# Optimization experiments

Hardware: AMD Instinct MI355X
Metric: run time of the kernel (lower is better)

The kernel has to match this reference:

```python
import jax, jax.numpy as jnp
import numpy as np

N, E, F, H, T, K = 50000, 800000, 128, 128, 10, 3


def setup_inputs() -> dict:
    key = jax.random.key(0)
    ks = jax.random.split(key, 12)
    def p(k, shape):
        return jax.random.normal(k, shape, dtype=jnp.float32) * 0.05
    inp = {
        "x": jax.random.normal(ks[0], (N, F), dtype=jnp.float32),
        "edge_index": jax.random.randint(ks[1], (2, E), 0, N, dtype=jnp.int64),
        "edge_weight": jax.random.uniform(ks[2], (E,), dtype=jnp.float32),
    }
    names = ["xz", "hz", "xr", "hr", "xh", "hh"]
    for i, nm in enumerate(names):
        cin = F if nm[0] == "x" else H
        inp["W" + nm] = p(ks[3 + i], (K, cin, H))  # ChebConv: K linear maps [in,out]
        inp["b" + nm] = jnp.zeros((H,), jnp.float32)
    inp["Wlin"] = p(ks[9], (H, T))
    inp["blin"] = jnp.zeros((T,), jnp.float32)
    return inp


def _cheb_norm(src, dst, edge_weight, n):
    # PyG ChebConv norm with normalization='sym', lambda_max=2.0:
    # L_hat = 2L/lambda_max - I = -D^{-1/2} A D^{-1/2}  (zero diagonal)
    deg = jax.ops.segment_sum(edge_weight, src, num_segments=n)
    deg_safe = jnp.where(deg > 0, deg, 1.0)
    dinv = jnp.where(deg > 0, jax.lax.rsqrt(deg_safe), 0.0)
    return -dinv[src] * edge_weight * dinv[dst]


def _cheb_conv(x, W, b, src, dst, norm, n):
    # out = sum_k T_k(L_hat) x @ W[k] + b, via Chebyshev recurrence
    def prop(t):  # L_hat @ t : gather from source nodes, scatter-add into targets
        return jax.ops.segment_sum(norm[:, None] * t[src], dst, num_segments=n)
    Tx0 = x
    out = Tx0 @ W[0]
    Tx1 = prop(Tx0)
    out = out + Tx1 @ W[1]
    for k in range(2, W.shape[0]):
        Tx2 = 2.0 * prop(Tx1) - Tx0
        out = out + Tx2 @ W[k]
        Tx0, Tx1 = Tx1, Tx2
    return out + b


def reference(x, edge_index, edge_weight, Wxz, bxz, Whz, bhz, Wxr, bxr,
              Whr, bhr, Wxh, bxh, Whh, bhh, Wlin, blin):
    n = x.shape[0]
    src, dst = edge_index[0], edge_index[1]
    norm = _cheb_norm(src, dst, edge_weight, n)
    Hs = jnp.zeros((n, Whz.shape[2]), x.dtype)  # GConvGRU inits H=None -> zeros
    Z = jax.nn.sigmoid(_cheb_conv(x, Wxz, bxz, src, dst, norm, n)
                       + _cheb_conv(Hs, Whz, bhz, src, dst, norm, n))
    R = jax.nn.sigmoid(_cheb_conv(x, Wxr, bxr, src, dst, norm, n)
                       + _cheb_conv(Hs, Whr, bhr, src, dst, norm, n))
    Ht = jnp.tanh(_cheb_conv(x, Wxh, bxh, src, dst, norm, n)
                  + _cheb_conv(Hs * R, Whh, bhh, src, dst, norm, n))
    Hn = Z * Hs + (1.0 - Z) * Ht
    return Hn @ Wlin + blin
```

## Files before the change

### kernel.cpp

```cpp
#include <hip/hip_runtime.h>

typedef __attribute__((ext_vector_type(8))) short bf16x8;
typedef __attribute__((ext_vector_type(4))) float f32x4;
typedef unsigned int u32;
typedef unsigned short u16;

#define CAP 48

static __device__ __forceinline__ u16 f2bf(float f) {
  u32 u = __float_as_uint(f);
  u32 r = (u + 0x7fffu + ((u >> 16) & 1u)) >> 16;
  return (u16)r;
}
static __device__ __forceinline__ void gload16(const void* g, void* l) {
  __builtin_amdgcn_global_load_lds((const __attribute__((address_space(1))) u32*)g,
                                   (__attribute__((address_space(3))) u32*)l, 16, 0, 0);
}

__global__ __launch_bounds__(256) void deg_kernel(const int* __restrict__ ei,
                                                  const float* __restrict__ w,
                                                  float* __restrict__ deg, int E, int N) {
  int e = blockIdx.x * 256 + threadIdx.x;
  if (e >= E) return;
  int s = ei[e];
  if ((unsigned)s < (unsigned)N) atomicAdd(&deg[s], w[e]);
}

__global__ __launch_bounds__(256) void scatter_kernel(const int* __restrict__ ei,
                                                      const float* __restrict__ w,
                                                      const float* __restrict__ deg,
                                                      int* __restrict__ cur,
                                                      int2* __restrict__ edges, int E, int N) {
  int e = blockIdx.x * 256 + threadIdx.x;
  if (e >= E) return;
  int s = ei[e], d = ei[E + e];
  if ((unsigned)s < (unsigned)N && (unsigned)d < (unsigned)N) {
    float ds = deg[s], dd = deg[d];
    float is = ds > 0.f ? rsqrtf(ds) : 0.f;
    float id = dd > 0.f ? rsqrtf(dd) : 0.f;
    float nv = -is * w[e] * id;
    int pos = atomicAdd(&cur[d], 1);
    if (pos < CAP) edges[d * CAP + pos] = make_int2(s, __float_as_int(nv));
  }
}

__global__ __launch_bounds__(256) void convert_kernel(const float* __restrict__ x,
                                                      u32* __restrict__ xw, int nw) {
  int i = blockIdx.x * 256 + threadIdx.x;
  if (i < nw) {
    float2 v = *(const float2*)&x[(size_t)i * 2];
    xw[i] = (u32)f2bf(v.x) | ((u32)f2bf(v.y) << 16);
  }
}

#define ACC8(VV, NN)                                                    \
  _Pragma("unroll") for (int k_ = 0; k_ < 8; ++k_) {                    \
    a0 += NN[k_] * __uint_as_float(VV[k_] << 16);                       \
    a1 += NN[k_] * __uint_as_float(VV[k_] & 0xffff0000u);               \
  }

__global__ __launch_bounds__(256) void prop1_kernel(const u32* __restrict__ xw,
    const int2* __restrict__ edges, const int* __restrict__ cur,
    u32* __restrict__ t1w, int N) {
  int node = (blockIdx.x << 2) + (threadIdx.x >> 6);
  if (node >= N) return;
  int lane = threadIdx.x & 63;
  int len = cur[node]; if (len > CAP) len = CAP;
  int2 my = edges[node * CAP + (lane < CAP ? lane : CAP - 1)];
  float a0 = 0.f, a1 = 0.f;
  u32 v[8]; float nv[8];
#pragma unroll
  for (int k = 0; k < 8; ++k) {
    int s = __shfl(my.x, k);
    float n = __int_as_float(__shfl(my.y, k));
    if (k < len) { v[k] = xw[((unsigned)s << 6) | (unsigned)lane]; nv[k] = n; }
    else { v[k] = 0; nv[k] = 0.f; }
  }
  for (int base = 0; base < len; base += 8) {
    u32 vv[8]; float nn[8];
#pragma unroll
    for (int k = 0; k < 8; ++k) { vv[k] = v[k]; nn[k] = nv[k]; }
#pragma unroll
    for (int k = 0; k < 8; ++k) {
      int kn = base + 8 + k;
      int s = __shfl(my.x, kn);
      float n = __int_as_float(__shfl(my.y, kn));
      if (kn < len) { v[k] = xw[((unsigned)s << 6) | (unsigned)lane]; nv[k] = n; }
      else { v[k] = 0; nv[k] = 0.f; }
    }
    ACC8(vv, nn);
  }
  t1w[((unsigned)node << 6) | (unsigned)lane] = (u32)f2bf(a0) | ((u32)f2bf(a1) << 16);
}

__global__ __launch_bounds__(256) void prop2_kernel(const u32* __restrict__ xbw,
    const u32* __restrict__ xw ,
    const int2* __restrict__ edges, const int* __restrict__ cur,
    u32* __restrict__ t2w, int N) {
  int node = (blockIdx.x << 2) + (threadIdx.x >> 6);
  if (node >= N) return;
  int lane = threadIdx.x & 63;
  int len = cur[node]; if (len > CAP) len = CAP;
  int2 my = edges[node * CAP + (lane < CAP ? lane : CAP - 1)];
  float a0 = 0.f, a1 = 0.f;
  u32 v[8]; float nv[8];
#pragma unroll
  for (int k = 0; k < 8; ++k) {
    int s = __shfl(my.x, k);
    float n = __int_as_float(__shfl(my.y, k));
    if (k < len) { v[k] = xw[((unsigned)s << 6) | (unsigned)lane]; nv[k] = n; }
    else { v[k] = 0; nv[k] = 0.f; }
  }
  for (int base = 0; base < len; base += 8) {
    u32 vv[8]; float nn[8];
#pragma unroll
    for (int k = 0; k < 8; ++k) { vv[k] = v[k]; nn[k] = nv[k]; }
#pragma unroll
    for (int k = 0; k < 8; ++k) {
      int kn = base + 8 + k;
      int s = __shfl(my.x, kn);
      float n = __int_as_float(__shfl(my.y, kn));
      if (kn < len) { v[k] = xw[((unsigned)s << 6) | (unsigned)lane]; nv[k] = n; }
      else { v[k] = 0; nv[k] = 0.f; }
    }
    ACC8(vv, nn);
  }
  u32 xv = xbw[((unsigned)node << 6) | (unsigned)lane];
  float r0 = 2.f * a0 - __uint_as_float(xv << 16);
  float r1 = 2.f * a1 - __uint_as_float(xv & 0xffff0000u);
  t2w[((unsigned)node << 6) | (unsigned)lane] = (u32)f2bf(r0) | ((u32)f2bf(r1) << 16);
}

__global__ __launch_bounds__(256) void packB_kernel(const float* __restrict__ Wxz,
    const float* __restrict__ Wxh, const float* __restrict__ bxz, const float* __restrict__ bhz,
    const float* __restrict__ bxh, const float* __restrict__ bhh,
    u16* __restrict__ Bp, float* __restrict__ bzs, float* __restrict__ bhs) {
  int idx = blockIdx.x * 256 + threadIdx.x;
  int j = idx & 7, h4 = (idx >> 3) & 3, n = (idx >> 5) & 15, ct = (idx >> 9) & 15, kt = idx >> 13;
  int k = kt * 32 + h4 * 8 + j;
  int c = ct * 16 + n;
  int kb = k >> 7, ci = k & 127, h = c >> 1;
  const float* W = (c & 1) ? Wxh : Wxz;
  float v = W[((size_t)kb * 128 + ci) * 128 + h];
  Bp[idx] = f2bf(v);
  if (idx < 128) { bzs[idx] = bxz[idx] + bhz[idx]; bhs[idx] = bxh[idx] + bhh[idx]; }
}

__global__ __launch_bounds__(512, 2) void gemm_kernel(
    const u16* __restrict__ xb, const u16* __restrict__ t1, const u16* __restrict__ t2,
    const u16* __restrict__ Bp, const float* __restrict__ bzs, const float* __restrict__ bhs,
    const float* __restrict__ Wlin, const float* __restrict__ blin,
    float* __restrict__ out, int N) {
  __shared__ __align__(16) char smem[49152];
  const int offB_[2] = {0, 16384};
  const int offA_[2] = {32768, 40960};

  int tid = threadIdx.x;
  int w = tid >> 6, lane = tid & 63;
  int l15 = lane & 15, lh = lane >> 4;
  int rowBase = blockIdx.x << 7;
  int wrow = (w >> 2) << 6;
  int wcol = (w & 3) << 6;

  const u16* acts[3] = {xb, t1, t2};

  f32x4 acc[4][4];
  f32x4 zero = {0.f, 0.f, 0.f, 0.f};
#pragma unroll
  for (int mi = 0; mi < 4; ++mi)
#pragma unroll
    for (int ni = 0; ni < 4; ++ni) acc[mi][ni] = zero;

  auto stageB = [&](int kt, int buf) {
    const char* g = (const char*)Bp + kt * 16384 + w * 2048 + lane * 16;
    char* l = smem + offB_[buf] + w * 2048;
    gload16(g, l);
    gload16(g + 1024, l + 1024);
  };
  auto stageA = [&](int kt, int buf) {
    int kb = kt >> 2;
    const u16* act = acts[kb];
    int rl = (w << 4) + (lane >> 2);
    int grow = rowBase + rl; if (grow >= N) grow = N - 1;
    int hsw = (lane & 3) ^ ((rl >> 1) & 3);
    const char* g = (const char*)act + (size_t)grow * 256 + ((kt & 3) << 6) + (hsw << 4);
    char* l = smem + offA_[buf] + (w << 10);
    gload16(g, l);
  };

  stageB(0, 0); stageA(0, 0);

#pragma unroll
  for (int kt = 0; kt < 12; ++kt) {
    __syncthreads();
    if (kt < 11) { stageB(kt + 1, (kt + 1) & 1); stageA(kt + 1, (kt + 1) & 1); }
    const char* Ab = smem + offA_[kt & 1];
    const char* Bb = smem + offB_[kt & 1];
    bf16x8 a[4], b[4];
#pragma unroll
    for (int mi = 0; mi < 4; ++mi) {
      int row = wrow + (mi << 4) + l15;
      int off = (row << 6) + ((lh ^ ((row >> 1) & 3)) << 4);
      a[mi] = *(const bf16x8*)(Ab + off);
    }
#pragma unroll
    for (int ni = 0; ni < 4; ++ni) {
      int ct = ((w & 3) << 2) + ni;
      int off = (((ct << 4) + l15) << 6) + (lh << 4);
      b[ni] = *(const bf16x8*)(Bb + off);
    }
#pragma unroll
    for (int mi = 0; mi < 4; ++mi)
#pragma unroll
      for (int ni = 0; ni < 4; ++ni)
        acc[mi][ni] = __builtin_amdgcn_mfma_f32_16x16x32_bf16(a[mi], b[ni], acc[mi][ni], 0, 0, 0);
  }

  __syncthreads();

  u16* HnS = (u16*)smem;
  float* WlS = (float*)(smem + 34816);
  float* blS = (float*)(smem + 34816 + 5120);
  for (int i = tid; i < 1280; i += 512) WlS[i] = Wlin[i];
  if (tid < 10) blS[tid] = blin[tid];

  int odd = lane & 1;
#pragma unroll
  for (int ni = 0; ni < 4; ++ni) {
    int h = (wcol + (ni << 4) + l15) >> 1;
    float badd = odd ? bhs[h] : bzs[h];
#pragma unroll
    for (int mi = 0; mi < 4; ++mi)
#pragma unroll
      for (int reg = 0; reg < 4; ++reg) {
        float pre = acc[mi][ni][reg] + badd;
        float s2 = odd ? 2.f * pre : pre;
        float e = __expf(s2);
        float A = odd ? 1.f : 0.f;
        float B = odd ? 2.f : -1.f;
        float r = A - B / (1.f + e);
        float o = __shfl_xor(r, 1);
        if (!odd) {
          int row = wrow + (mi << 4) + (lh << 2) + reg;
          HnS[row * 136 + h] = f2bf(r * o);
        }
      }
  }
  __syncthreads();

  for (int idx = tid; idx < 1280; idx += 512) {
    int row = idx / 10, t = idx - row * 10;
    int grow = rowBase + row;
    if (grow < N) {
      float s = blS[t];
      const u16* hr = HnS + row * 136;
#pragma unroll 4
      for (int hc = 0; hc < 16; ++hc) {
        uint4 q = *(const uint4*)(hr + (hc << 3));
        const float* wp = WlS + (hc << 3) * 10 + t;
        s += __uint_as_float(q.x << 16) * wp[0];
        s += __uint_as_float(q.x & 0xffff0000u) * wp[10];
        s += __uint_as_float(q.y << 16) * wp[20];
        s += __uint_as_float(q.y & 0xffff0000u) * wp[30];
        s += __uint_as_float(q.z << 16) * wp[40];
        s += __uint_as_float(q.z & 0xffff0000u) * wp[50];
        s += __uint_as_float(q.w << 16) * wp[60];
        s += __uint_as_float(q.w & 0xffff0000u) * wp[70];
      }
      out[(size_t)grow * 10 + t] = s;
    }
  }
}

extern "C" void kernel_launch(void* const* d_in, const int* in_sizes, int n_in,
                              void* d_out, int out_size, void* d_ws, size_t ws_size,
                              hipStream_t stream) {
  const float* x    = (const float*)d_in[0];
  const int*   ei   = (const int*)d_in[1];
  const float* w    = (const float*)d_in[2];
  const float* Wxz  = (const float*)d_in[3];
  const float* bxz  = (const float*)d_in[4];
  const float* bhz  = (const float*)d_in[6];
  const float* Wxh  = (const float*)d_in[11];
  const float* bxh  = (const float*)d_in[12];
  const float* bhh  = (const float*)d_in[14];
  const float* Wlin = (const float*)d_in[15];
  const float* blin = (const float*)d_in[16];
  float* out = (float*)d_out;

  int N = in_sizes[0] / 128;
  int E = in_sizes[2];

  char* p = (char*)d_ws;
  auto alloc = [&](size_t bytes) {
    char* r = p;
    p += (bytes + 255) & ~(size_t)255;
    return r;
  };
  float* deg   = (float*)alloc((size_t)N * 4);
  int*   cur   = (int*)alloc((size_t)N * 4);
  int2*  edges = (int2*)alloc((size_t)N * CAP * 8);
  u32*   xbw   = (u32*)alloc((size_t)N * 256);
  u32*   t1w   = (u32*)alloc((size_t)N * 256);
  u32*   t2w   = (u32*)alloc((size_t)N * 256);
  u16*   Bp    = (u16*)alloc(196608);
  float* bzs   = (float*)alloc(512);
  float* bhs   = (float*)alloc(512);

  hipMemsetAsync(deg, 0, (size_t)N * 4, stream);
  hipMemsetAsync(cur, 0, (size_t)N * 4, stream);

  int eb = (E + 255) / 256;
  int nw = N * 64;
  hipLaunchKernelGGL(convert_kernel, dim3((nw + 255) / 256), dim3(256), 0, stream, x, xbw, nw);
  hipLaunchKernelGGL(packB_kernel, dim3(384), dim3(256), 0, stream,
                     Wxz, Wxh, bxz, bhz, bxh, bhh, Bp, bzs, bhs);
  hipLaunchKernelGGL(deg_kernel, dim3(eb), dim3(256), 0, stream, ei, w, deg, E, N);
  hipLaunchKernelGGL(scatter_kernel, dim3(eb), dim3(256), 0, stream, ei, w, deg, cur, edges, E, N);
  int nb = (N + 3) / 4;
  hipLaunchKernelGGL(prop1_kernel, dim3(nb), dim3(256), 0, stream, xbw, edges, cur, t1w, N);
  hipLaunchKernelGGL(prop2_kernel, dim3(nb), dim3(256), 0, stream, xbw, t1w, edges, cur, t2w, N);
  int gb = (N + 127) / 128;
  hipLaunchKernelGGL(gemm_kernel, dim3(gb), dim3(512), 0, stream,
                     (const u16*)xbw, (const u16*)t1w, (const u16*)t2w, Bp, bzs, bhs,
                     Wlin, blin, out, N);
}
```

Before: 297.6 us.

## Fuse preprocessing into one kernel and factor degree normalization out of edges

Merges the convert, weight-pack, degree and edge-scatter kernels into a single launch, interleaving roles by block index so the degree and scatter passes no longer run serially. The symmetric normalization is factored out of the edge weights: node features are pre-scaled by D^-1/2 and the other D^-1/2 is applied after aggregation. That lets each edge record pack the source id and an fp16 raw weight into 32 bits, halving edge storage. Propagation unroll grows from 8 to 16 neighbours for more loads in flight. The cost is an extra scale pass and extra stored arrays. The 17-bit node index limit and the fp16 weight add precision and range risk.

```diff
diff --git a/kernel.cpp b/kernel.cpp
--- a/kernel.cpp
+++ b/kernel.cpp
@@ -1,4 +1,5 @@
 #include <hip/hip_runtime.h>
+#include <hip/hip_fp16.h>
 
 typedef __attribute__((ext_vector_type(8))) short bf16x8;
 typedef __attribute__((ext_vector_type(4))) float f32x4;
@@ -12,138 +13,163 @@
   u32 r = (u + 0x7fffu + ((u >> 16) & 1u)) >> 16;
   return (u16)r;
 }
+static __device__ __forceinline__ u32 f2h15(float f) {
+  __half h = __float2half(f);
+  return (u32)(((__half_raw)h).x) & 0x7FFFu;
+}
+static __device__ __forceinline__ float h152f(u32 b) {
+  __half_raw hr; hr.x = (u16)b;
+  return __half2float(__half(hr));
+}
 static __device__ __forceinline__ void gload16(const void* g, void* l) {
   __builtin_amdgcn_global_load_lds((const __attribute__((address_space(1))) u32*)g,
                                    (__attribute__((address_space(3))) u32*)l, 16, 0, 0);
 }
 
-__global__ __launch_bounds__(256) void deg_kernel(const int* __restrict__ ei,
-                                                  const float* __restrict__ w,
-                                                  float* __restrict__ deg, int E, int N) {
-  int e = blockIdx.x * 256 + threadIdx.x;
-  if (e >= E) return;
-  int s = ei[e];
-  if ((unsigned)s < (unsigned)N) atomicAdd(&deg[s], w[e]);
-}
-
-__global__ __launch_bounds__(256) void scatter_kernel(const int* __restrict__ ei,
-                                                      const float* __restrict__ w,
-                                                      const float* __restrict__ deg,
-                                                      int* __restrict__ cur,
-                                                      int2* __restrict__ edges, int E, int N) {
-  int e = blockIdx.x * 256 + threadIdx.x;
-  if (e >= E) return;
-  int s = ei[e], d = ei[E + e];
-  if ((unsigned)s < (unsigned)N && (unsigned)d < (unsigned)N) {
-    float ds = deg[s], dd = deg[d];
-    float is = ds > 0.f ? rsqrtf(ds) : 0.f;
-    float id = dd > 0.f ? rsqrtf(dd) : 0.f;
-    float nv = -is * w[e] * id;
-    int pos = atomicAdd(&cur[d], 1);
-    if (pos < CAP) edges[d * CAP + pos] = make_int2(s, __float_as_int(nv));
-  }
-}
-
-__global__ __launch_bounds__(256) void convert_kernel(const float* __restrict__ x,
-                                                      u32* __restrict__ xw, int nw) {
-  int i = blockIdx.x * 256 + threadIdx.x;
-  if (i < nw) {
-    float2 v = *(const float2*)&x[(size_t)i * 2];
-    xw[i] = (u32)f2bf(v.x) | ((u32)f2bf(v.y) << 16);
-  }
-}
-
-#define ACC8(VV, NN)                                                    \
-  _Pragma("unroll") for (int k_ = 0; k_ < 8; ++k_) {                    \
+__global__ __launch_bounds__(256) void mega_kernel(
+    const float* __restrict__ x, const int* __restrict__ ei, const float* __restrict__ w,
+    const float* __restrict__ Wxz, const float* __restrict__ Wxh,
+    const float* __restrict__ bxz, const float* __restrict__ bhz,
+    const float* __restrict__ bxh, const float* __restrict__ bhh,
+    u32* __restrict__ xw, float* __restrict__ deg, int* __restrict__ cur,
+    u32* __restrict__ edges, u16* __restrict__ Bp, float* __restrict__ bzs,
+    float* __restrict__ bhs, int E, int N, int nw, int eb, int pbBase, int interleave) {
+  int bid = blockIdx.x, tid = threadIdx.x;
+  if (bid >= pbBase) {
+    int idx = (bid - pbBase) * 256 + tid;
+    int j = idx & 7, h4 = (idx >> 3) & 3, n = (idx >> 5) & 15, ct = (idx >> 9) & 15, kt = idx >> 13;
+    int k = kt * 32 + h4 * 8 + j;
+    int c = ct * 16 + n;
+    int kb = k >> 7, ci = k & 127, h = c >> 1;
+    const float* W = (c & 1) ? Wxh : Wxz;
+    float v = W[((size_t)kb * 128 + ci) * 128 + h];
+    Bp[idx] = f2bf(v);
+    if (idx < 128) { bzs[idx] = bxz[idx] + bhz[idx]; bhs[idx] = bxh[idx] + bhh[idx]; }
+    return;
+  }
+  int role, g;
+  if (interleave) { int r = bid % 6; g = bid / 6; role = (r >= 2) ? 2 : r; if (r >= 2) g = g * 4 + (r - 2); }
+  else { if (bid < eb) { role = 0; g = bid; } else if (bid < 2 * eb) { role = 1; g = bid - eb; } else { role = 2; g = bid - 2 * eb; } }
+
+  if (role == 2) {
+    int i = g * 256 + tid;
+    if (i < nw) {
+      float2 v = *(const float2*)&x[(size_t)i * 2];
+      xw[i] = (u32)f2bf(v.x) | ((u32)f2bf(v.y) << 16);
+    }
+  } else if (role == 0) {
+    int e = g * 256 + tid;
+    if (e < E) {
+      int s = ei[e];
+      if ((unsigned)s < (unsigned)N) atomicAdd(&deg[s], w[e]);
+    }
+  } else {
+    int e = g * 256 + tid;
+    if (e < E) {
+      int s = ei[e], d = ei[E + e];
+      if ((unsigned)s < (unsigned)N && (unsigned)d < (unsigned)N) {
+        u32 rec = ((u32)s << 15) | f2h15(w[e]);
+        int pos = atomicAdd(&cur[d], 1);
+        if (pos < CAP) edges[d * CAP + pos] = rec;
+      }
+    }
+  }
+}
+
+__global__ __launch_bounds__(256) void scale_kernel(const u32* __restrict__ xw,
+                                                    const float* __restrict__ deg,
+                                                    u32* __restrict__ xs, int N) {
+  int node = (blockIdx.x << 2) + (threadIdx.x >> 6);
+  if (node >= N) return;
+  int lane = threadIdx.x & 63;
+  float dd = deg[node];
+  float di = dd > 0.f ? rsqrtf(dd) : 0.f;
+  u32 v = xw[((unsigned)node << 6) | (unsigned)lane];
+  float f0 = di * __uint_as_float(v << 16);
+  float f1 = di * __uint_as_float(v & 0xffff0000u);
+  xs[((unsigned)node << 6) | (unsigned)lane] = (u32)f2bf(f0) | ((u32)f2bf(f1) << 16);
+}
+
+#define ACC16(VV, NN)                                                   \
+  _Pragma("unroll") for (int k_ = 0; k_ < 16; ++k_) {                   \
     a0 += NN[k_] * __uint_as_float(VV[k_] << 16);                       \
     a1 += NN[k_] * __uint_as_float(VV[k_] & 0xffff0000u);               \
   }
 
-__global__ __launch_bounds__(256) void prop1_kernel(const u32* __restrict__ xw,
-    const int2* __restrict__ edges, const int* __restrict__ cur,
-    u32* __restrict__ t1w, int N) {
+__global__ __launch_bounds__(256) void prop1_kernel(const u32* __restrict__ xs,
+    const float* __restrict__ deg, const u32* __restrict__ edges, const int* __restrict__ cur,
+    u32* __restrict__ t1w, u32* __restrict__ t1s, int N) {
   int node = (blockIdx.x << 2) + (threadIdx.x >> 6);
   if (node >= N) return;
   int lane = threadIdx.x & 63;
   int len = cur[node]; if (len > CAP) len = CAP;
-  int2 my = edges[node * CAP + (lane < CAP ? lane : CAP - 1)];
+  u32 my = edges[node * CAP + (lane < CAP ? lane : CAP - 1)];
   float a0 = 0.f, a1 = 0.f;
-  u32 v[8]; float nv[8];
-#pragma unroll
-  for (int k = 0; k < 8; ++k) {
-    int s = __shfl(my.x, k);
-    float n = __int_as_float(__shfl(my.y, k));
-    if (k < len) { v[k] = xw[((unsigned)s << 6) | (unsigned)lane]; nv[k] = n; }
+  u32 v[16]; float nv[16];
+#pragma unroll
+  for (int k = 0; k < 16; ++k) {
+    u32 rec = (u32)__shfl((int)my, k);
+    if (k < len) { v[k] = xs[((rec >> 15) << 6) | (unsigned)lane]; nv[k] = h152f(rec & 0x7FFFu); }
     else { v[k] = 0; nv[k] = 0.f; }
   }
-  for (int base = 0; base < len; base += 8) {
-    u32 vv[8]; float nn[8];
-#pragma unroll
-    for (int k = 0; k < 8; ++k) { vv[k] = v[k]; nn[k] = nv[k]; }
-#pragma unroll
-    for (int k = 0; k < 8; ++k) {
-      int kn = base + 8 + k;
-      int s = __shfl(my.x, kn);
-      float n = __int_as_float(__shfl(my.y, kn));
-      if (kn < len) { v[k] = xw[((unsigned)s << 6) | (unsigned)lane]; nv[k] = n; }
+  for (int base = 0; base < len; base += 16) {
+    u32 vv[16]; float nn[16];
+#pragma unroll
+    for (int k = 0; k < 16; ++k) { vv[k] = v[k]; nn[k] = nv[k]; }
+#pragma unroll
+    for (int k = 0; k < 16; ++k) {
+      int kn = base + 16 + k;
+      u32 rec = (u32)__shfl((int)my, kn);
+      if (kn < len) { v[k] = xs[((rec >> 15) << 6) | (unsigned)lane]; nv[k] = h152f(rec & 0x7FFFu); }
       else { v[k] = 0; nv[k] = 0.f; }
     }
-    ACC8(vv, nn);
-  }
-  t1w[((unsigned)node << 6) | (unsigned)lane] = (u32)f2bf(a0) | ((u32)f2bf(a1) << 16);
-}
-
-__global__ __launch_bounds__(256) void prop2_kernel(const u32* __restrict__ xbw,
-    const u32* __restrict__ xw ,
-    const int2* __restrict__ edges, const int* __restrict__ cur,
+    ACC16(vv, nn);
+  }
+  float dd = deg[node];
+  float di = dd > 0.f ? rsqrtf(dd) : 0.f;
+  float T0 = -di * a0, T1 = -di * a1;
+  unsigned idx = ((unsigned)node << 6) | (unsigned)lane;
+  t1w[idx] = (u32)f2bf(T0) | ((u32)f2bf(T1) << 16);
+  t1s[idx] = (u32)f2bf(di * T0) | ((u32)f2bf(di * T1) << 16);
+}
+
+__global__ __launch_bounds__(256) void prop2_kernel(const u32* __restrict__ xw,
+    const u32* __restrict__ t1s, const float* __restrict__ deg,
+    const u32* __restrict__ edges, const int* __restrict__ cur,
     u32* __restrict__ t2w, int N) {
   int node = (blockIdx.x << 2) + (threadIdx.x >> 6);
   if (node >= N) return;
   int lane = threadIdx.x & 63;
   int len = cur[node]; if (len > CAP) len = CAP;
-  int2 my = edges[node * CAP + (lane < CAP ? lane : CAP - 1)];
+  u32 my = edges[node * CAP + (lane < CAP ? lane : CAP - 1)];
   float a0 = 0.f, a1 = 0.f;
-  u32 v[8]; float nv[8];
-#pragma unroll
-  for (int k = 0; k < 8; ++k) {
-    int s = __shfl(my.x, k);
-    float n = __int_as_float(__shfl(my.y, k));
-    if (k < len) { v[k] = xw[((unsigned)s << 6) | (unsigned)lane]; nv[k] = n; }
+  u32 v[16]; float nv[16];
+#pragma unroll
+  for (int k = 0; k < 16; ++k) {
+    u32 rec = (u32)__shfl((int)my, k);
+    if (k < len) { v[k] = t1s[((rec >> 15) << 6) | (unsigned)lane]; nv[k] = h152f(rec & 0x7FFFu); }
     else { v[k] = 0; nv[k] = 0.f; }
   }
-  for (int base = 0; base < len; base += 8) {
-    u32 vv[8]; float nn[8];
-#pragma unroll
-    for (int k = 0; k < 8; ++k) { vv[k] = v[k]; nn[k] = nv[k]; }
-#pragma unroll
-    for (int k = 0; k < 8; ++k) {
-      int kn = base + 8 + k;
-      int s = __shfl(my.x, kn);
-      float n = __int_as_float(__shfl(my.y, kn));
-      if (kn < len) { v[k] = xw[((unsigned)s << 6) | (unsigned)lane]; nv[k] = n; }
+  for (int base = 0; base < len; base += 16) {
+    u32 vv[16]; float nn[16];
+#pragma unroll
+    for (int k = 0; k < 16; ++k) { vv[k] = v[k]; nn[k] = nv[k]; }
+#pragma unroll
+    for (int k = 0; k < 16; ++k) {
+      int kn = base + 16 + k;
+      u32 rec = (u32)__shfl((int)my, kn);
+      if (kn < len) { v[k] = t1s[((rec >> 15) << 6) | (unsigned)lane]; nv[k] = h152f(rec & 0x7FFFu); }
       else { v[k] = 0; nv[k] = 0.f; }
     }
-    ACC8(vv, nn);
-  }
-  u32 xv = xbw[((unsigned)node << 6) | (unsigned)lane];
-  float r0 = 2.f * a0 - __uint_as_float(xv << 16);
-  float r1 = 2.f * a1 - __uint_as_float(xv & 0xffff0000u);
-  t2w[((unsigned)node << 6) | (unsigned)lane] = (u32)f2bf(r0) | ((u32)f2bf(r1) << 16);
-}
-
-__global__ __launch_bounds__(256) void packB_kernel(const float* __restrict__ Wxz,
-    const float* __restrict__ Wxh, const float* __restrict__ bxz, const float* __restrict__ bhz,
-    const float* __restrict__ bxh, const float* __restrict__ bhh,
-    u16* __restrict__ Bp, float* __restrict__ bzs, float* __restrict__ bhs) {
-  int idx = blockIdx.x * 256 + threadIdx.x;
-  int j = idx & 7, h4 = (idx >> 3) & 3, n = (idx >> 5) & 15, ct = (idx >> 9) & 15, kt = idx >> 13;
-  int k = kt * 32 + h4 * 8 + j;
-  int c = ct * 16 + n;
-  int kb = k >> 7, ci = k & 127, h = c >> 1;
-  const float* W = (c & 1) ? Wxh : Wxz;
-  float v = W[((size_t)kb * 128 + ci) * 128 + h];
-  Bp[idx] = f2bf(v);
-  if (idx < 128) { bzs[idx] = bxz[idx] + bhz[idx]; bhs[idx] = bxh[idx] + bhh[idx]; }
+    ACC16(vv, nn);
+  }
+  float dd = deg[node];
+  float di = dd > 0.f ? rsqrtf(dd) : 0.f;
+  unsigned idx = ((unsigned)node << 6) | (unsigned)lane;
+  u32 xv = xw[idx];
+  float r0 = -2.f * di * a0 - __uint_as_float(xv << 16);
+  float r1 = -2.f * di * a1 - __uint_as_float(xv & 0xffff0000u);
+  t2w[idx] = (u32)f2bf(r0) | ((u32)f2bf(r1) << 16);
 }
 
 __global__ __launch_bounds__(512, 2) void gemm_kernel(
@@ -299,9 +325,11 @@
   };
   float* deg   = (float*)alloc((size_t)N * 4);
   int*   cur   = (int*)alloc((size_t)N * 4);
-  int2*  edges = (int2*)alloc((size_t)N * CAP * 8);
+  u32*   edges = (u32*)alloc((size_t)N * CAP * 4);
   u32*   xbw   = (u32*)alloc((size_t)N * 256);
+  u32*   xs    = (u32*)alloc((size_t)N * 256);
   u32*   t1w   = (u32*)alloc((size_t)N * 256);
+  u32*   t1s   = (u32*)alloc((size_t)N * 256);
   u32*   t2w   = (u32*)alloc((size_t)N * 256);
   u16*   Bp    = (u16*)alloc(196608);
   float* bzs   = (float*)alloc(512);
@@ -310,16 +338,21 @@
   hipMemsetAsync(deg, 0, (size_t)N * 4, stream);
   hipMemsetAsync(cur, 0, (size_t)N * 4, stream);
 
+  int nw = N * 64;
   int eb = (E + 255) / 256;
-  int nw = N * 64;
-  hipLaunchKernelGGL(convert_kernel, dim3((nw + 255) / 256), dim3(256), 0, stream, x, xbw, nw);
-  hipLaunchKernelGGL(packB_kernel, dim3(384), dim3(256), 0, stream,
-                     Wxz, Wxh, bxz, bhz, bxh, bhh, Bp, bzs, bhs);
-  hipLaunchKernelGGL(deg_kernel, dim3(eb), dim3(256), 0, stream, ei, w, deg, E, N);
-  hipLaunchKernelGGL(scatter_kernel, dim3(eb), dim3(256), 0, stream, ei, w, deg, cur, edges, E, N);
+  int cb = (nw + 255) / 256;
+  int interleave = (cb == 4 * eb) ? 1 : 0;
+  int workB = interleave ? 6 * eb : (2 * eb + cb);
+  int pbBase = workB;
+  int grid = workB + 384;
+
+  hipLaunchKernelGGL(mega_kernel, dim3(grid), dim3(256), 0, stream,
+                     x, ei, w, Wxz, Wxh, bxz, bhz, bxh, bhh,
+                     xbw, deg, cur, edges, Bp, bzs, bhs, E, N, nw, eb, pbBase, interleave);
   int nb = (N + 3) / 4;
-  hipLaunchKernelGGL(prop1_kernel, dim3(nb), dim3(256), 0, stream, xbw, edges, cur, t1w, N);
-  hipLaunchKernelGGL(prop2_kernel, dim3(nb), dim3(256), 0, stream, xbw, t1w, edges, cur, t2w, N);
+  hipLaunchKernelGGL(scale_kernel, dim3(nb), dim3(256), 0, stream, xbw, deg, xs, N);
+  hipLaunchKernelGGL(prop1_kernel, dim3(nb), dim3(256), 0, stream, xs, deg, edges, cur, t1w, t1s, N);
+  hipLaunchKernelGGL(prop2_kernel, dim3(nb), dim3(256), 0, stream, xbw, t1s, deg, edges, cur, t2w, N);
   int gb = (N + 127) / 128;
   hipLaunchKernelGGL(gemm_kernel, dim3(gb), dim3(512), 0, stream,
                      (const u16*)xbw, (const u16*)t1w, (const u16*)t2w, Bp, bzs, bhs,
```

Measured after the change: 295.5 us. Within noise of the previous version (-0.7%).
